# Kernel optimization log

Measured on AMD Instinct MI355X. Metric: run time of the kernel, lower is better.

The kernel has to match this reference:

```python
import jax, jax.numpy as jnp
import numpy as np

B, NSIDE, NH = 4, 64, 8
N = 12 * NSIDE * NSIDE          # HEALPix pixel count, nested ordering
CIN, CHID, COUT = 256, 512, 256
WS = 16                          # window = 4**(w+1) nested pixels, w=1
HD = CHID // NH


def _ln(x, g, b, eps=1e-5):
    m = x.mean(-1, keepdims=True)
    v = ((x - m) ** 2).mean(-1, keepdims=True)
    return (x - m) * jax.lax.rsqrt(v + eps) * g + b


def _win_attn(x, qkv_w, qkv_b, pw, pb):
    b_, n_, c = x.shape
    nw = n_ // WS
    xw = x.reshape(b_, nw, WS, c)
    qkv = xw @ qkv_w + qkv_b                      # [B, nw, ws, 3C]
    q, k, v = jnp.split(qkv, 3, axis=-1)
    def heads(t):
        return t.reshape(b_, nw, WS, NH, HD).transpose(0, 1, 3, 2, 4)
    q, k, v = heads(q), heads(k), heads(v)        # [B, nw, H, ws, hd]
    a = jax.nn.softmax(jnp.einsum('bwhqd,bwhkd->bwhqk', q, k) * (HD ** -0.5), axis=-1)
    o = jnp.einsum('bwhqk,bwhkd->bwhqd', a, v)
    o = o.transpose(0, 1, 3, 2, 4).reshape(b_, n_, c)
    return o @ pw + pb


def _heal_block(x, p, shift):
    if shift:
        x = jnp.roll(x, -WS // 2, axis=1)          # shifted-window (cyclic in nested order)
    x = x + _win_attn(_ln(x, p['ln1g'], p['ln1b']), p['qkvw'], p['qkvb'], p['pw'], p['pb'])
    h = _ln(x, p['ln2g'], p['ln2b'])
    h = jax.nn.gelu(h @ p['m1w'] + p['m1b'], approximate=False) @ p['m2w'] + p['m2b']
    x = x + h
    if shift:
        x = jnp.roll(x, WS // 2, axis=1)
    return x


def _sn_linear(h, W, b, u):
    # torch spectral_norm: one power-iteration, u/v detached, sigma = u' W v
    v = W @ u                                      # [CHID]
    v = jax.lax.stop_gradient(v / (jnp.linalg.norm(v) + 1e-12))
    u2 = v @ W                                     # [COUT]
    u2 = jax.lax.stop_gradient(u2 / (jnp.linalg.norm(u2) + 1e-12))
    sigma = v @ W @ u2
    return h @ (W / sigma) + b


def setup_inputs() -> dict:
    key = jax.random.key(0)
    ks = iter(jax.random.split(key, 64))
    def w(shape, s=0.02):
        return jax.random.normal(next(ks), shape, jnp.float32) * s
    inp = {'x': jax.random.normal(next(ks), (B, N, CIN), jnp.float32)}
    inp['ff1_w'] = w((CIN, CHID)); inp['ff1_b'] = jnp.zeros((CHID,), jnp.float32)
    for pre in ('a', 'b'):
        inp[f'{pre}_ln1g'] = jnp.ones((CHID,), jnp.float32)
        inp[f'{pre}_ln1b'] = jnp.zeros((CHID,), jnp.float32)
        inp[f'{pre}_qkvw'] = w((CHID, 3 * CHID)); inp[f'{pre}_qkvb'] = jnp.zeros((3 * CHID,), jnp.float32)
        inp[f'{pre}_pw'] = w((CHID, CHID)); inp[f'{pre}_pb'] = jnp.zeros((CHID,), jnp.float32)
        inp[f'{pre}_ln2g'] = jnp.ones((CHID,), jnp.float32)
        inp[f'{pre}_ln2b'] = jnp.zeros((CHID,), jnp.float32)
        inp[f'{pre}_m1w'] = w((CHID, 4 * CHID)); inp[f'{pre}_m1b'] = jnp.zeros((4 * CHID,), jnp.float32)
        inp[f'{pre}_m2w'] = w((4 * CHID, CHID)); inp[f'{pre}_m2b'] = jnp.zeros((CHID,), jnp.float32)
    inp['ff2_w'] = w((CHID, COUT)); inp['ff2_b'] = jnp.zeros((COUT,), jnp.float32)
    inp['ff2_u'] = jax.random.normal(next(ks), (COUT,), jnp.float32)
    return inp


def reference(x, ff1_w, ff1_b,
              a_ln1g, a_ln1b, a_qkvw, a_qkvb, a_pw, a_pb, a_ln2g, a_ln2b, a_m1w, a_m1b, a_m2w, a_m2b,
              b_ln1g, b_ln1b, b_qkvw, b_qkvb, b_pw, b_pb, b_ln2g, b_ln2b, b_m1w, b_m1b, b_m2w, b_m2b,
              ff2_w, ff2_b, ff2_u):
    pa = dict(ln1g=a_ln1g, ln1b=a_ln1b, qkvw=a_qkvw, qkvb=a_qkvb, pw=a_pw, pb=a_pb,
              ln2g=a_ln2g, ln2b=a_ln2b, m1w=a_m1w, m1b=a_m1b, m2w=a_m2w, m2b=a_m2b)
    pb_ = dict(ln1g=b_ln1g, ln1b=b_ln1b, qkvw=b_qkvw, qkvb=b_qkvb, pw=b_pw, pb=b_pb,
               ln2g=b_ln2g, ln2b=b_ln2b, m1w=b_m1w, m1b=b_m1b, m2w=b_m2w, m2b=b_m2b)
    h = jax.nn.gelu(x @ ff1_w + ff1_b, approximate=False)   # feed_forward1
    h = _heal_block(h, pa, shift=False)                     # message_passing1
    h = _heal_block(h, pb_, shift=True)                     # message_passing2
    return _sn_linear(h, ff2_w, ff2_b, ff2_u)               # spectral-norm linear
```

## Files before the change

### kernel.cpp

```cpp
#include <hip/hip_runtime.h>
#include <hip/hip_bf16.h>
#include <math.h>

typedef _Float16 f16;
typedef __attribute__((ext_vector_type(8))) _Float16 f16x8;
typedef __attribute__((ext_vector_type(4))) _Float16 f16x4;
typedef __attribute__((ext_vector_type(4))) float f32x4;

#define DINLINE __device__ __forceinline__

DINLINE float gelu_fast(float x) {
  float x2 = x * x;
  float z = x * __builtin_fmaf(-0.10294537f, x2, -2.30211422f);
  float E = __builtin_amdgcn_exp2f(z);
  return x * __builtin_amdgcn_rcpf(1.0f + E);
}
DINLINE void gload16(const void* g, void* l) {
  __builtin_amdgcn_global_load_lds((const __attribute__((address_space(1))) void*)g,
                                   (__attribute__((address_space(3))) void*)l, 16, 0, 0);
}

#define BAR       __builtin_amdgcn_s_barrier()
#define WAITVM(n) asm volatile("s_waitcnt vmcnt(" #n ")" ::: "memory")
#define CFE       asm volatile("" ::: "memory")

template <int EPI>
__global__ __launch_bounds__(512, 4) void gemm(
    const f16* __restrict__ A, const f16* __restrict__ Bt,
    const float* __restrict__ bias, const f16* __restrict__ Cin,
    float* __restrict__ Cf, f16* __restrict__ Cb,
    const float* __restrict__ scale_ptr,
    int N, int K, int nct)
{
  __shared__ alignas(16) f16 smf[2 * 3 * 4096];

  const int nwg = (int)gridDim.x;
  const int gid = (int)blockIdx.x;
  const int q = nwg >> 3, r = nwg & 7;
  const int xcd = gid & 7, idx = gid >> 3;
  const int swz = (xcd < r ? xcd * (q + 1) : r * (q + 1) + (xcd - r) * q) + idx;
  const int rt = swz / nct, ct = swz - rt * nct;
  const int m0 = rt << 7, n0 = ct << 8;

  const int tid = (int)threadIdx.x;
  const int lane = tid & 63;
  const int wid = tid >> 6;
  const int wr = wid >> 2, wcn = wid & 3;

  const int rsel = lane & 15, khi = lane >> 4;
  const int sx = (khi ^ ((rsel >> 1) & 3)) << 3;

  const int srow = tid >> 2;
  const int sls = (tid & 3) ^ ((srow >> 1) & 3);
  const f16* pA  = A  + (size_t)(m0 + srow) * K + sls * 8;
  const f16* pB0 = Bt + (size_t)(n0 + srow) * K + sls * 8;
  const f16* pB1 = Bt + (size_t)(n0 + 128 + srow) * K + sls * 8;
  f16* ldst = smf + tid * 8;

  const int aB = (wr * 64 + rsel) * 32 + sx;
  const int bB = (1 + (wcn >> 1)) * 4096 + ((wcn & 1) * 64 + rsel) * 32 + sx;

  f32x4 acc[4][4] = {};
  const int NT = K >> 5;

#define STG(boff)                                                             \
  {                                                                           \
    gload16(pA,  ldst + (boff));                                              \
    gload16(pB0, ldst + (boff) + 4096);                                       \
    gload16(pB1, ldst + (boff) + 8192);                                       \
    pA += 32; pB0 += 32; pB1 += 32;                                           \
  }

#define CMP(boff)                                                             \
  {                                                                           \
    f16x8 aF[4], bF[4];                                                       \
    _Pragma("unroll")                                                         \
    for (int _i = 0; _i < 4; ++_i)                                            \
      aF[_i] = *(const f16x8*)(smf + (boff) + aB + _i * 512);                 \
    _Pragma("unroll")                                                         \
    for (int _i = 0; _i < 4; ++_i)                                            \
      bF[_i] = *(const f16x8*)(smf + (boff) + bB + _i * 512);                 \
    __builtin_amdgcn_s_setprio(1);                                            \
    _Pragma("unroll")                                                         \
    for (int _m = 0; _m < 4; ++_m)                                            \
      _Pragma("unroll")                                                       \
      for (int _n = 0; _n < 4; ++_n)                                          \
        acc[_m][_n] = __builtin_amdgcn_mfma_f32_16x16x32_f16(                 \
            bF[_n], aF[_m], acc[_m][_n], 0, 0, 0);                            \
    __builtin_amdgcn_s_setprio(0);                                            \
  }

  STG(0); STG(12288);
  for (int t = 0; t + 2 < NT; t += 2) {
    WAITVM(3); BAR; CFE;
    CMP(0);
    BAR; CFE;
    STG(0);
    WAITVM(3); BAR; CFE;
    CMP(12288);
    BAR; CFE;
    STG(12288);
  }
  WAITVM(3); BAR; CFE;
  CMP(0);
  BAR; CFE;
  WAITVM(0); BAR; CFE;
  CMP(12288);

  const float scale = (EPI & 8) ? scale_ptr[0] : 1.0f;
  const int R0 = m0 + wr * 64, C0 = n0 + wcn * 64;
#pragma unroll
  for (int m = 0; m < 4; ++m) {
    const int row = R0 + m * 16 + rsel;
#pragma unroll
    for (int n = 0; n < 4; ++n) {
      const int col = C0 + n * 16 + (khi << 2);
      f32x4 v = acc[m][n];
      if (EPI & 8) {
#pragma unroll
        for (int j = 0; j < 4; ++j) v[j] *= scale;
      }
      f32x4 bb = *(const f32x4*)(bias + col);
#pragma unroll
      for (int j = 0; j < 4; ++j) v[j] += bb[j];
      if (EPI & 1) {
#pragma unroll
        for (int j = 0; j < 4; ++j) v[j] = gelu_fast(v[j]);
      }
      if (EPI & 2) {
        f16x4 c4 = *(const f16x4*)(Cin + (size_t)row * N + col);
#pragma unroll
        for (int j = 0; j < 4; ++j) v[j] += (float)c4[j];
      }
      if (EPI & 4) {
        f16x4 o;
#pragma unroll
        for (int j = 0; j < 4; ++j) o[j] = (f16)v[j];
        *(f16x4*)(Cb + (size_t)row * N + col) = o;
      } else {
        *(f32x4*)(Cf + (size_t)row * N + col) = v;
      }
    }
  }
#undef STG
#undef CMP
}

__global__ __launch_bounds__(256) void ln_f16(
    const f16* __restrict__ X, const float* __restrict__ g,
    const float* __restrict__ b, f16* __restrict__ Y, int ntok)
{
  const int lane = threadIdx.x & 63;
  const int c = lane * 8;
  const f32x4 g0 = *(const f32x4*)(g + c), g1 = *(const f32x4*)(g + c + 4);
  const f32x4 b0 = *(const f32x4*)(b + c), b1 = *(const f32x4*)(b + c + 4);
  for (int token = blockIdx.x * 4 + (threadIdx.x >> 6); token < ntok;
       token += gridDim.x * 4) {
    f16x8 v = *(const f16x8*)(X + (size_t)token * 512 + c);
    float vf[8];
    float s = 0.f, s2 = 0.f;
#pragma unroll
    for (int j = 0; j < 8; ++j) { vf[j] = (float)v[j]; s += vf[j]; s2 += vf[j] * vf[j]; }
#pragma unroll
    for (int o = 32; o > 0; o >>= 1) { s += __shfl_xor(s, o, 64); s2 += __shfl_xor(s2, o, 64); }
    const float mean = s * (1.f / 512.f);
    const float inv = rsqrtf(s2 * (1.f / 512.f) - mean * mean + 1e-5f);
    f16x8 o8;
#pragma unroll
    for (int j = 0; j < 4; ++j) {
      o8[j]     = (f16)((vf[j] - mean) * inv * g0[j] + b0[j]);
      o8[4 + j] = (f16)((vf[4 + j] - mean) * inv * g1[j] + b1[j]);
    }
    *(f16x8*)(Y + (size_t)token * 512 + c) = o8;
  }
}

__global__ __launch_bounds__(256) void cvt_f32_f16(const float* __restrict__ X,
                                                   f16* __restrict__ Y, long n8)
{
  const long i = (long)blockIdx.x * 256 + threadIdx.x;
  if (i >= n8) return;
  f32x4 v0 = *(const f32x4*)(X + i * 8), v1 = *(const f32x4*)(X + i * 8 + 4);
  f16x8 o8;
#pragma unroll
  for (int j = 0; j < 4; ++j) { o8[j] = (f16)v0[j]; o8[4 + j] = (f16)v1[j]; }
  *(f16x8*)(Y + i * 8) = o8;
}

__global__ __launch_bounds__(256) void w_tr_tiled(const float* __restrict__ W,
                                                  f16* __restrict__ Wt, int K, int N)
{
  __shared__ f16 td[64][66];
  const int nkt = K >> 6;
  const int kt = blockIdx.x % nkt, nt = blockIdx.x / nkt;
  const int k0 = kt << 6, n0 = nt << 6;
  const int col = threadIdx.x & 63, rq = threadIdx.x >> 6;
#pragma unroll
  for (int j = 0; j < 16; ++j) {
    const int row = j * 4 + rq;
    td[row][col] = (f16)W[(size_t)(k0 + row) * N + n0 + col];
  }
  __syncthreads();
#pragma unroll
  for (int j = 0; j < 16; ++j) {
    const int nrow = j * 4 + rq;
    Wt[(size_t)(n0 + nrow) * K + k0 + col] = td[col][nrow];
  }
}

template <int SHIFT>
__global__ __launch_bounds__(256) void win_attn(const f16* __restrict__ QKV,
                                                f16* __restrict__ O)
{
  __shared__ alignas(16) f16 kv[2][16][1160];
  const int wl0 = (int)blockIdx.x * 2;
  const int tid = (int)threadIdx.x;

  for (int i = tid; i < 4096; i += 256) {
    const int win = i >> 11;
    const int rem = i & 2047;
    const int row = rem >> 7;
    const int c8 = rem & 127;
    const int src = ((wl0 + win) * 16 + row + SHIFT) % 49152;
    const int sect = c8 >> 6;
    const int hh = (c8 >> 3) & 7;
    const int dd = (c8 & 7) * 8;
    *(f16x8*)(&kv[win][row][sect * 576 + hh * 72 + dd]) =
        *(const f16x8*)(QKV + (size_t)src * 1536 + 512 + c8 * 8);
  }

  const int win = tid >> 7, h = (tid >> 4) & 7, qi = tid & 15;
  const int qtok = ((wl0 + win) * 16 + qi + SHIFT) % 49152;
  f16x8 qv[8];
#pragma unroll
  for (int c8 = 0; c8 < 8; ++c8)
    qv[c8] = *(const f16x8*)(QKV + (size_t)qtok * 1536 + h * 64 + c8 * 8);

  __syncthreads();

  float sc[16];
  float mx = -1e30f;
#pragma unroll
  for (int kj = 0; kj < 16; ++kj) {
    const f16* kr = &kv[win][kj][h * 72];
    float s = 0.f;
#pragma unroll
    for (int c8 = 0; c8 < 8; ++c8) {
      f16x8 k8 = *(const f16x8*)(kr + c8 * 8);
#pragma unroll
      for (int j = 0; j < 8; ++j) s += (float)qv[c8][j] * (float)k8[j];
    }
    s *= 0.125f;
    sc[kj] = s;
    mx = fmaxf(mx, s);
  }
  float sum = 0.f;
#pragma unroll
  for (int kj = 0; kj < 16; ++kj) { sc[kj] = expf(sc[kj] - mx); sum += sc[kj]; }
  const float inv = 1.f / sum;
  float ov[64] = {};
#pragma unroll
  for (int kj = 0; kj < 16; ++kj) {
    const float a = sc[kj] * inv;
    const f16* vr = &kv[win][kj][576 + h * 72];
#pragma unroll
    for (int c8 = 0; c8 < 8; ++c8) {
      f16x8 v8 = *(const f16x8*)(vr + c8 * 8);
#pragma unroll
      for (int j = 0; j < 8; ++j) ov[c8 * 8 + j] += a * (float)v8[j];
    }
  }
  f16* orow = O + (size_t)qtok * 512 + h * 64;
#pragma unroll
  for (int c8 = 0; c8 < 8; ++c8) {
    f16x8 t;
#pragma unroll
    for (int j = 0; j < 8; ++j) t[j] = (f16)ov[c8 * 8 + j];
    *(f16x8*)(orow + c8 * 8) = t;
  }
}

__global__ __launch_bounds__(256) void sn_sigma(const float* __restrict__ W,
                                                const float* __restrict__ u,
                                                float* __restrict__ inv_sigma)
{
  __shared__ float vsh[512];
  __shared__ float ush[256];
  __shared__ float red[256];
  const int t = (int)threadIdx.x;
  ush[t] = u[t];
  __syncthreads();
  float a0 = 0.f, a1 = 0.f;
  for (int j = 0; j < 256; ++j) {
    a0 += W[t * 256 + j] * ush[j];
    a1 += W[(t + 256) * 256 + j] * ush[j];
  }
  vsh[t] = a0; vsh[t + 256] = a1;
  red[t] = a0 * a0 + a1 * a1;
  __syncthreads();
  for (int s = 128; s > 0; s >>= 1) { if (t < s) red[t] += red[t + s]; __syncthreads(); }
  const float nv = sqrtf(red[0]) + 1e-12f;
  __syncthreads();
  const float invv = 1.f / nv;
  vsh[t] *= invv; vsh[t + 256] *= invv;
  __syncthreads();
  float u2 = 0.f;
  for (int i = 0; i < 512; ++i) u2 += vsh[i] * W[i * 256 + t];
  red[t] = u2 * u2;
  __syncthreads();
  for (int s = 128; s > 0; s >>= 1) { if (t < s) red[t] += red[t + s]; __syncthreads(); }
  const float nu = sqrtf(red[0]) + 1e-12f;
  __syncthreads();
  ush[t] = u2 / nu;
  __syncthreads();
  float d0 = 0.f, d1 = 0.f;
  for (int j = 0; j < 256; ++j) {
    d0 += W[t * 256 + j] * ush[j];
    d1 += W[(t + 256) * 256 + j] * ush[j];
  }
  red[t] = vsh[t] * d0 + vsh[t + 256] * d1;
  __syncthreads();
  for (int s = 128; s > 0; s >>= 1) { if (t < s) red[t] += red[t + s]; __syncthreads(); }
  if (t == 0) inv_sigma[0] = 1.f / red[0];
}

__global__ void fill_sentinel(float* __restrict__ out, long n, float val)
{
  const long i = (long)blockIdx.x * 256 + threadIdx.x;
  for (long k = i; k < n; k += (long)gridDim.x * 256) out[k] = val;
}

extern "C" void kernel_launch(void* const* d_in, const int* in_sizes, int n_in,
                              void* d_out, int out_size, void* d_ws, size_t ws_size,
                              hipStream_t stream)
{
  const int M = 196608;
  const int MC = 49152;
  constexpr size_t OFF_U   = 201326592ull;
  constexpr size_t OFF_OH  = 201326592ull + 150994944ull;
  constexpr size_t OFF_WT  = 402653184ull;
  constexpr size_t OFF_SIG = 415760384ull;
  constexpr size_t NEED    = OFF_SIG + 256ull;

  if (ws_size < NEED) {
    fill_sentinel<<<2048, 256, 0, stream>>>((float*)d_out, (long)out_size,
                                            (float)(ws_size >> 20));
    return;
  }

  char* ws = (char*)d_ws;
  f16* R     = (f16*)(ws);
  f16* U     = (f16*)(ws + OFF_U);
  f16* OH    = (f16*)(ws + OFF_OH);
  f16* WT    = (f16*)(ws + OFF_WT);
  float* sig = (float*)(ws + OFF_SIG);
  f16* X     = (f16*)d_out;

  const float* ff1_b = (const float*)d_in[2];
  const float* ff2_b = (const float*)d_in[28];

  f16* W_FF1 = WT;
  auto W_QKV = [&](int blk) { return WT + (blk ? 3276800 : 131072); };
  auto W_PW  = [&](int blk) { return WT + (blk ? 4063232 : 917504); };
  auto W_M1  = [&](int blk) { return WT + (blk ? 4325376 : 1179648); };
  auto W_M2  = [&](int blk) { return WT + (blk ? 5373952 : 2228224); };
  f16* W_FF2 = WT + 6422528;

  w_tr_tiled<<<32, 256, 0, stream>>>((const float*)d_in[1], W_FF1, 256, 512);
  for (int blk = 0; blk < 2; ++blk) {
    w_tr_tiled<<<192, 256, 0, stream>>>((const float*)d_in[blk ? 17 : 5], W_QKV(blk), 512, 1536);
    w_tr_tiled<<<64, 256, 0, stream>>>((const float*)d_in[blk ? 19 : 7], W_PW(blk), 512, 512);
    w_tr_tiled<<<256, 256, 0, stream>>>((const float*)d_in[blk ? 23 : 11], W_M1(blk), 512, 2048);
    w_tr_tiled<<<256, 256, 0, stream>>>((const float*)d_in[blk ? 25 : 13], W_M2(blk), 2048, 512);
  }
  w_tr_tiled<<<32, 256, 0, stream>>>((const float*)d_in[27], W_FF2, 512, 256);
  sn_sigma<<<1, 256, 0, stream>>>((const float*)d_in[27], (const float*)d_in[29], sig);

  cvt_f32_f16<<<24576, 256, 0, stream>>>((const float*)d_in[0], U, (long)M * 256 / 8);
  gemm<5><<<3072, 512, 0, stream>>>(U, W_FF1, ff1_b, nullptr, nullptr, R, nullptr,
                                    512, 256, 2);

  for (int blk = 0; blk < 2; ++blk) {
    const float* ln1g = (const float*)d_in[blk ? 15 : 3];
    const float* ln1b = (const float*)d_in[blk ? 16 : 4];
    const float* qkvb = (const float*)d_in[blk ? 18 : 6];
    const float* pb   = (const float*)d_in[blk ? 20 : 8];
    const float* ln2g = (const float*)d_in[blk ? 21 : 9];
    const float* ln2b = (const float*)d_in[blk ? 22 : 10];
    const float* m1b  = (const float*)d_in[blk ? 24 : 12];
    const float* m2b  = (const float*)d_in[blk ? 26 : 14];

    ln_f16<<<4096, 256, 0, stream>>>(R, ln1g, ln1b, X, M);
    for (int mc = 0; mc < 4; ++mc) {
      const size_t ro = (size_t)mc * MC * 512;
      gemm<4><<<2304, 512, 0, stream>>>(X + ro, W_QKV(blk), qkvb, nullptr,
                                        nullptr, U, nullptr, 1536, 512, 6);
      if (blk == 0) win_attn<0><<<1536, 256, 0, stream>>>(U, OH);
      else          win_attn<8><<<1536, 256, 0, stream>>>(U, OH);
      gemm<6><<<768, 512, 0, stream>>>(OH, W_PW(blk), pb, R + ro,
                                       nullptr, R + ro, nullptr, 512, 512, 2);
    }
    ln_f16<<<4096, 256, 0, stream>>>(R, ln2g, ln2b, X, M);
    for (int mc = 0; mc < 4; ++mc) {
      const size_t ro = (size_t)mc * MC * 512;
      gemm<5><<<3072, 512, 0, stream>>>(X + ro, W_M1(blk), m1b, nullptr,
                                        nullptr, U, nullptr, 2048, 512, 8);
      gemm<6><<<768, 512, 0, stream>>>(U, W_M2(blk), m2b, R + ro,
                                       nullptr, R + ro, nullptr, 512, 2048, 2);
    }
  }

  gemm<8><<<1536, 512, 0, stream>>>(R, W_FF2, ff2_b, nullptr, (float*)d_out,
                                    nullptr, sig, 256, 512, 1);
}
```

Baseline: 4.794 ms.

## Fold LayerNorm into following GEMMs via row stats and precomputed weight sums

Replaces the LayerNorm kernels that wrote a normalized f16 copy of the activations with a stats-only kernel that stores per-token inv-std and mean*inv. The LN gain is folded into the transposed weights, and the GEMM epilogue applies inv*acc - mean*inv*colsum(gW) plus a folded bias (b + lnb@W). This removes a full activation write and re-read per LayerNorm. The risk is precision: the GEMM now runs on un-normalized f16 inputs and subtracts the mean afterwards, which can cancel when mean is large relative to variance.

```diff
diff --git a/kernel.cpp b/kernel.cpp
--- a/kernel.cpp
+++ b/kernel.cpp
@@ -6,6 +6,7 @@
 typedef __attribute__((ext_vector_type(8))) _Float16 f16x8;
 typedef __attribute__((ext_vector_type(4))) _Float16 f16x4;
 typedef __attribute__((ext_vector_type(4))) float f32x4;
+typedef __attribute__((ext_vector_type(2))) float f32x2;
 
 #define DINLINE __device__ __forceinline__
 
@@ -30,6 +31,7 @@
     const float* __restrict__ bias, const f16* __restrict__ Cin,
     float* __restrict__ Cf, f16* __restrict__ Cb,
     const float* __restrict__ scale_ptr,
+    const float* __restrict__ stats, const float* __restrict__ svec,
     int N, int K, int nct)
 {
   __shared__ alignas(16) f16 smf[2 * 3 * 4096];
@@ -112,6 +114,11 @@
 #pragma unroll
   for (int m = 0; m < 4; ++m) {
     const int row = R0 + m * 16 + rsel;
+    float inv = 1.0f, muinv = 0.0f;
+    if (EPI & 16) {
+      f32x2 sld = *(const f32x2*)(stats + (row << 1));
+      inv = sld[0]; muinv = sld[1];
+    }
 #pragma unroll
     for (int n = 0; n < 4; ++n) {
       const int col = C0 + n * 16 + (khi << 2);
@@ -119,6 +126,12 @@
       if (EPI & 8) {
 #pragma unroll
         for (int j = 0; j < 4; ++j) v[j] *= scale;
+      }
+      if (EPI & 16) {
+        f32x4 sv = *(const f32x4*)(svec + col);
+#pragma unroll
+        for (int j = 0; j < 4; ++j)
+          v[j] = __builtin_fmaf(inv, v[j], -muinv * sv[j]);
       }
       f32x4 bb = *(const f32x4*)(bias + col);
 #pragma unroll
@@ -146,32 +159,49 @@
 #undef CMP
 }
 
-__global__ __launch_bounds__(256) void ln_f16(
-    const f16* __restrict__ X, const float* __restrict__ g,
-    const float* __restrict__ b, f16* __restrict__ Y, int ntok)
+__global__ __launch_bounds__(256) void ln_stats(
+    const f16* __restrict__ X, float* __restrict__ st, int ntok)
 {
   const int lane = threadIdx.x & 63;
-  const int c = lane * 8;
-  const f32x4 g0 = *(const f32x4*)(g + c), g1 = *(const f32x4*)(g + c + 4);
-  const f32x4 b0 = *(const f32x4*)(b + c), b1 = *(const f32x4*)(b + c + 4);
   for (int token = blockIdx.x * 4 + (threadIdx.x >> 6); token < ntok;
        token += gridDim.x * 4) {
-    f16x8 v = *(const f16x8*)(X + (size_t)token * 512 + c);
-    float vf[8];
+    f16x8 v = *(const f16x8*)(X + (size_t)token * 512 + lane * 8);
     float s = 0.f, s2 = 0.f;
 #pragma unroll
-    for (int j = 0; j < 8; ++j) { vf[j] = (float)v[j]; s += vf[j]; s2 += vf[j] * vf[j]; }
+    for (int j = 0; j < 8; ++j) { float f = (float)v[j]; s += f; s2 += f * f; }
 #pragma unroll
     for (int o = 32; o > 0; o >>= 1) { s += __shfl_xor(s, o, 64); s2 += __shfl_xor(s2, o, 64); }
-    const float mean = s * (1.f / 512.f);
-    const float inv = rsqrtf(s2 * (1.f / 512.f) - mean * mean + 1e-5f);
-    f16x8 o8;
-#pragma unroll
-    for (int j = 0; j < 4; ++j) {
-      o8[j]     = (f16)((vf[j] - mean) * inv * g0[j] + b0[j]);
-      o8[4 + j] = (f16)((vf[4 + j] - mean) * inv * g1[j] + b1[j]);
-    }
-    *(f16x8*)(Y + (size_t)token * 512 + c) = o8;
+    if (lane == 0) {
+      const float mean = s * (1.f / 512.f);
+      const float inv = rsqrtf(s2 * (1.f / 512.f) - mean * mean + 1e-5f);
+      f32x2 o2; o2[0] = inv; o2[1] = mean * inv;
+      *(f32x2*)(st + 2 * (size_t)token) = o2;
+    }
+  }
+}
+
+__global__ __launch_bounds__(256) void prep_svec(
+    const float* __restrict__ W, const float* __restrict__ g,
+    const float* __restrict__ lb, const float* __restrict__ b0,
+    float* __restrict__ s, float* __restrict__ bout, int K, int N)
+{
+  __shared__ float red[2][4][64];
+  const int c = threadIdx.x & 63;
+  const int n = blockIdx.x * 64 + c;
+  const int kc = threadIdx.x >> 6;
+  const int kpc = K >> 2;
+  float ps = 0.f, pt = 0.f;
+  for (int k = kc * kpc; k < (kc + 1) * kpc; ++k) {
+    float w = W[(size_t)k * N + n];
+    ps += g[k] * w;
+    pt += lb[k] * w;
+  }
+  red[0][kc][c] = ps;
+  red[1][kc][c] = pt;
+  __syncthreads();
+  if (kc == 0) {
+    s[n] = red[0][0][c] + red[0][1][c] + red[0][2][c] + red[0][3][c];
+    bout[n] = b0[n] + red[1][0][c] + red[1][1][c] + red[1][2][c] + red[1][3][c];
   }
 }
 
@@ -188,6 +218,7 @@
 }
 
 __global__ __launch_bounds__(256) void w_tr_tiled(const float* __restrict__ W,
+                                                  const float* __restrict__ gain,
                                                   f16* __restrict__ Wt, int K, int N)
 {
   __shared__ f16 td[64][66];
@@ -198,7 +229,8 @@
 #pragma unroll
   for (int j = 0; j < 16; ++j) {
     const int row = j * 4 + rq;
-    td[row][col] = (f16)W[(size_t)(k0 + row) * N + n0 + col];
+    const float gv = gain ? gain[k0 + row] : 1.0f;
+    td[row][col] = (f16)(W[(size_t)(k0 + row) * N + n0 + col] * gv);
   }
   __syncthreads();
 #pragma unroll
@@ -354,7 +386,13 @@
   f16* OH    = (f16*)(ws + OFF_OH);
   f16* WT    = (f16*)(ws + OFF_WT);
   float* sig = (float*)(ws + OFF_SIG);
-  f16* X     = (f16*)d_out;
+
+  float* ST = (float*)d_out;
+  float* SV = ST + 393216;
+  auto SQ  = [&](int blk) { return SV + blk * 7168; };
+  auto BQ  = [&](int blk) { return SV + blk * 7168 + 1536; };
+  auto SM1 = [&](int blk) { return SV + blk * 7168 + 3072; };
+  auto BM1 = [&](int blk) { return SV + blk * 7168 + 5120; };
 
   const float* ff1_b = (const float*)d_in[2];
   const float* ff2_b = (const float*)d_in[28];
@@ -366,50 +404,60 @@
   auto W_M2  = [&](int blk) { return WT + (blk ? 5373952 : 2228224); };
   f16* W_FF2 = WT + 6422528;
 
-  w_tr_tiled<<<32, 256, 0, stream>>>((const float*)d_in[1], W_FF1, 256, 512);
+  w_tr_tiled<<<32, 256, 0, stream>>>((const float*)d_in[1], nullptr, W_FF1, 256, 512);
   for (int blk = 0; blk < 2; ++blk) {
-    w_tr_tiled<<<192, 256, 0, stream>>>((const float*)d_in[blk ? 17 : 5], W_QKV(blk), 512, 1536);
-    w_tr_tiled<<<64, 256, 0, stream>>>((const float*)d_in[blk ? 19 : 7], W_PW(blk), 512, 512);
-    w_tr_tiled<<<256, 256, 0, stream>>>((const float*)d_in[blk ? 23 : 11], W_M1(blk), 512, 2048);
-    w_tr_tiled<<<256, 256, 0, stream>>>((const float*)d_in[blk ? 25 : 13], W_M2(blk), 2048, 512);
-  }
-  w_tr_tiled<<<32, 256, 0, stream>>>((const float*)d_in[27], W_FF2, 512, 256);
-  sn_sigma<<<1, 256, 0, stream>>>((const float*)d_in[27], (const float*)d_in[29], sig);
-
-  cvt_f32_f16<<<24576, 256, 0, stream>>>((const float*)d_in[0], U, (long)M * 256 / 8);
-  gemm<5><<<3072, 512, 0, stream>>>(U, W_FF1, ff1_b, nullptr, nullptr, R, nullptr,
-                                    512, 256, 2);
-
-  for (int blk = 0; blk < 2; ++blk) {
+    const float* qkvw = (const float*)d_in[blk ? 17 : 5];
+    const float* m1w  = (const float*)d_in[blk ? 23 : 11];
     const float* ln1g = (const float*)d_in[blk ? 15 : 3];
     const float* ln1b = (const float*)d_in[blk ? 16 : 4];
     const float* qkvb = (const float*)d_in[blk ? 18 : 6];
-    const float* pb   = (const float*)d_in[blk ? 20 : 8];
     const float* ln2g = (const float*)d_in[blk ? 21 : 9];
     const float* ln2b = (const float*)d_in[blk ? 22 : 10];
     const float* m1b  = (const float*)d_in[blk ? 24 : 12];
-    const float* m2b  = (const float*)d_in[blk ? 26 : 14];
-
-    ln_f16<<<4096, 256, 0, stream>>>(R, ln1g, ln1b, X, M);
+    w_tr_tiled<<<192, 256, 0, stream>>>(qkvw, ln1g, W_QKV(blk), 512, 1536);
+    w_tr_tiled<<<64, 256, 0, stream>>>((const float*)d_in[blk ? 19 : 7], nullptr, W_PW(blk), 512, 512);
+    w_tr_tiled<<<256, 256, 0, stream>>>(m1w, ln2g, W_M1(blk), 512, 2048);
+    w_tr_tiled<<<256, 256, 0, stream>>>((const float*)d_in[blk ? 25 : 13], nullptr, W_M2(blk), 2048, 512);
+    prep_svec<<<24, 256, 0, stream>>>(qkvw, ln1g, ln1b, qkvb, SQ(blk), BQ(blk), 512, 1536);
+    prep_svec<<<32, 256, 0, stream>>>(m1w, ln2g, ln2b, m1b, SM1(blk), BM1(blk), 512, 2048);
+  }
+  w_tr_tiled<<<32, 256, 0, stream>>>((const float*)d_in[27], nullptr, W_FF2, 512, 256);
+  sn_sigma<<<1, 256, 0, stream>>>((const float*)d_in[27], (const float*)d_in[29], sig);
+
+  cvt_f32_f16<<<24576, 256, 0, stream>>>((const float*)d_in[0], U, (long)M * 256 / 8);
+  gemm<5><<<3072, 512, 0, stream>>>(U, W_FF1, ff1_b, nullptr, nullptr, R, nullptr,
+                                    nullptr, nullptr, 512, 256, 2);
+
+  for (int blk = 0; blk < 2; ++blk) {
+    const float* pb  = (const float*)d_in[blk ? 20 : 8];
+    const float* m2b = (const float*)d_in[blk ? 26 : 14];
+
+    ln_stats<<<4096, 256, 0, stream>>>(R, ST, M);
     for (int mc = 0; mc < 4; ++mc) {
       const size_t ro = (size_t)mc * MC * 512;
-      gemm<4><<<2304, 512, 0, stream>>>(X + ro, W_QKV(blk), qkvb, nullptr,
-                                        nullptr, U, nullptr, 1536, 512, 6);
+      gemm<20><<<2304, 512, 0, stream>>>(R + ro, W_QKV(blk), BQ(blk), nullptr,
+                                         nullptr, U, nullptr,
+                                         ST + 2 * (size_t)mc * MC, SQ(blk),
+                                         1536, 512, 6);
       if (blk == 0) win_attn<0><<<1536, 256, 0, stream>>>(U, OH);
       else          win_attn<8><<<1536, 256, 0, stream>>>(U, OH);
       gemm<6><<<768, 512, 0, stream>>>(OH, W_PW(blk), pb, R + ro,
-                                       nullptr, R + ro, nullptr, 512, 512, 2);
-    }
-    ln_f16<<<4096, 256, 0, stream>>>(R, ln2g, ln2b, X, M);
+                                       nullptr, R + ro, nullptr,
+                                       nullptr, nullptr, 512, 512, 2);
+    }
+    ln_stats<<<4096, 256, 0, stream>>>(R, ST, M);
     for (int mc = 0; mc < 4; ++mc) {
       const size_t ro = (size_t)mc * MC * 512;
-      gemm<5><<<3072, 512, 0, stream>>>(X + ro, W_M1(blk), m1b, nullptr,
-                                        nullptr, U, nullptr, 2048, 512, 8);
+      gemm<21><<<3072, 512, 0, stream>>>(R + ro, W_M1(blk), BM1(blk), nullptr,
+                                         nullptr, U, nullptr,
+                                         ST + 2 * (size_t)mc * MC, SM1(blk),
+                                         2048, 512, 8);
       gemm<6><<<768, 512, 0, stream>>>(U, W_M2(blk), m2b, R + ro,
-                                       nullptr, R + ro, nullptr, 512, 2048, 2);
+                                       nullptr, R + ro, nullptr,
+                                       nullptr, nullptr, 512, 2048, 2);
     }
   }
 
   gemm<8><<<1536, 512, 0, stream>>>(R, W_FF2, ff2_b, nullptr, (float*)d_out,
-                                    nullptr, sig, 256, 512, 1);
-}
+                                    nullptr, sig, nullptr, nullptr, 256, 512, 1);
+}
```

Result: slower. 5.022 ms (+4.8%).

## Fuse MLP up-projection, GELU and down-projection into one kernel

Applied to the files above, without the earlier changes.

Replaces the per-chunk pair of GEMMs (m1 with GELU writing a 2048-wide hidden buffer, then m2 with residual add) with a single fused_mlp kernel. Each workgroup owns 128 rows and loops over 16 hidden slabs of 128. For each slab it computes the GELU hidden tile into LDS and immediately accumulates it into a 128x512 output accumulator. This removes the global round-trip of the large hidden activation and the extra launches. In exchange it uses 128KB of LDS and a large register accumulator at occupancy 1, with 1536 workgroups and less latency hiding.

```diff
diff --git a/kernel.cpp b/kernel.cpp
--- a/kernel.cpp
+++ b/kernel.cpp
@@ -21,8 +21,33 @@
 }
 
 #define BAR       __builtin_amdgcn_s_barrier()
+#define WAITLGKM  asm volatile("s_waitcnt lgkmcnt(0)" ::: "memory")
 #define WAITVM(n) asm volatile("s_waitcnt vmcnt(" #n ")" ::: "memory")
 #define CFE       asm volatile("" ::: "memory")
+
+#define EPILOG(vreg, rowE, colE)                                              \
+  {                                                                           \
+    f32x4 v = (vreg);                                                         \
+    if (EPI & 8) {                                                            \
+      _Pragma("unroll") for (int _j = 0; _j < 4; ++_j) v[_j] *= scale;        \
+    }                                                                         \
+    f32x4 bb = *(const f32x4*)(bias + (colE));                                \
+    _Pragma("unroll") for (int _j = 0; _j < 4; ++_j) v[_j] += bb[_j];         \
+    if (EPI & 1) {                                                            \
+      _Pragma("unroll") for (int _j = 0; _j < 4; ++_j) v[_j] = gelu_fast(v[_j]); \
+    }                                                                         \
+    if (EPI & 2) {                                                            \
+      f16x4 c4 = *(const f16x4*)(Cin + (size_t)(rowE) * N + (colE));          \
+      _Pragma("unroll") for (int _j = 0; _j < 4; ++_j) v[_j] += (float)c4[_j];\
+    }                                                                         \
+    if (EPI & 4) {                                                            \
+      f16x4 o;                                                                \
+      _Pragma("unroll") for (int _j = 0; _j < 4; ++_j) o[_j] = (f16)v[_j];    \
+      *(f16x4*)(Cb + (size_t)(rowE) * N + (colE)) = o;                        \
+    } else {                                                                  \
+      *(f32x4*)(Cf + (size_t)(rowE) * N + (colE)) = v;                        \
+    }                                                                         \
+  }
 
 template <int EPI>
 __global__ __launch_bounds__(512, 4) void gemm(
@@ -50,11 +75,11 @@
   const int rsel = lane & 15, khi = lane >> 4;
   const int sx = (khi ^ ((rsel >> 1) & 3)) << 3;
 
-  const int srow = tid >> 2;
-  const int sls = (tid & 3) ^ ((srow >> 1) & 3);
-  const f16* pA  = A  + (size_t)(m0 + srow) * K + sls * 8;
-  const f16* pB0 = Bt + (size_t)(n0 + srow) * K + sls * 8;
-  const f16* pB1 = Bt + (size_t)(n0 + 128 + srow) * K + sls * 8;
+  const int r0 = tid >> 2;
+  const int sls = (tid & 3) ^ ((r0 >> 1) & 3);
+  const f16* pA  = A  + (size_t)(m0 + r0) * K + sls * 8;
+  const f16* pB0 = Bt + (size_t)(n0 + r0) * K + sls * 8;
+  const f16* pB1 = Bt + (size_t)(n0 + 128 + r0) * K + sls * 8;
   f16* ldst = smf + tid * 8;
 
   const int aB = (wr * 64 + rsel) * 32 + sx;
@@ -115,35 +140,155 @@
 #pragma unroll
     for (int n = 0; n < 4; ++n) {
       const int col = C0 + n * 16 + (khi << 2);
-      f32x4 v = acc[m][n];
-      if (EPI & 8) {
-#pragma unroll
-        for (int j = 0; j < 4; ++j) v[j] *= scale;
-      }
-      f32x4 bb = *(const f32x4*)(bias + col);
-#pragma unroll
-      for (int j = 0; j < 4; ++j) v[j] += bb[j];
-      if (EPI & 1) {
-#pragma unroll
-        for (int j = 0; j < 4; ++j) v[j] = gelu_fast(v[j]);
-      }
-      if (EPI & 2) {
-        f16x4 c4 = *(const f16x4*)(Cin + (size_t)row * N + col);
-#pragma unroll
-        for (int j = 0; j < 4; ++j) v[j] += (float)c4[j];
-      }
-      if (EPI & 4) {
-        f16x4 o;
-#pragma unroll
-        for (int j = 0; j < 4; ++j) o[j] = (f16)v[j];
-        *(f16x4*)(Cb + (size_t)row * N + col) = o;
-      } else {
-        *(f32x4*)(Cf + (size_t)row * N + col) = v;
-      }
+      EPILOG(acc[m][n], row, col);
     }
   }
 #undef STG
 #undef CMP
+}
+
+__global__ __launch_bounds__(512, 1) void fused_mlp(
+    const f16* __restrict__ X, const f16* __restrict__ W1t,
+    const float* __restrict__ b1, const f16* __restrict__ W2t,
+    const float* __restrict__ b2, f16* __restrict__ R)
+{
+  __shared__ alignas(16) f16 lds[65536];
+
+  const int nwg = (int)gridDim.x;
+  const int gid = (int)blockIdx.x;
+  const int m0 = ((gid & 7) * (nwg >> 3) + (gid >> 3)) << 7;
+
+  const int tid = (int)threadIdx.x;
+  const int lane = tid & 63;
+  const int wid = tid >> 6;
+  const int wr = wid >> 2;
+  const int wq = wid & 3;
+  const int rsel = lane & 15, khi = lane >> 4;
+  const int sx = (khi ^ ((rsel >> 1) & 3)) << 3;
+
+  const int srow = tid >> 2;
+  const int sls = (tid & 3) ^ ((srow >> 1) & 3);
+
+  f32x4 acc2[4][8] = {};
+
+#define STG1(boff, ktv)                                                       \
+  {                                                                           \
+    gload16(X + (size_t)(m0 + srow) * 512 + (ktv) * 32 + sls * 8,             \
+            lds + (boff) + tid * 8);                                          \
+    gload16(W1t + (size_t)(hbase + srow) * 512 + (ktv) * 32 + sls * 8,        \
+            lds + 8192 + (boff) + tid * 8);                                   \
+  }
+
+#define STG2(boff, kt2v)                                                      \
+  {                                                                           \
+    _Pragma("unroll")                                                         \
+    for (int _rg = 0; _rg < 4; ++_rg)                                         \
+      gload16(W2t + (size_t)(_rg * 128 + srow) * 2048 + hbase + (kt2v) * 32 + sls * 8, \
+              lds + 32768 + (boff) + _rg * 4096 + tid * 8);                   \
+  }
+
+#define CMP1(boff)                                                            \
+  {                                                                           \
+    f16x8 xF[4], wF[2];                                                       \
+    _Pragma("unroll") for (int _i = 0; _i < 4; ++_i)                          \
+      xF[_i] = *(const f16x8*)(lds + (boff) + (wr * 64 + _i * 16 + rsel) * 32 + sx); \
+    _Pragma("unroll") for (int _j = 0; _j < 2; ++_j)                          \
+      wF[_j] = *(const f16x8*)(lds + 8192 + (boff) + (wq * 32 + _j * 16 + rsel) * 32 + sx); \
+    __builtin_amdgcn_s_setprio(1);                                            \
+    _Pragma("unroll") for (int _i = 0; _i < 4; ++_i)                          \
+      _Pragma("unroll") for (int _j = 0; _j < 2; ++_j)                        \
+        acc1[_i][_j] = __builtin_amdgcn_mfma_f32_16x16x32_f16(                \
+            wF[_j], xF[_i], acc1[_i][_j], 0, 0, 0);                           \
+    __builtin_amdgcn_s_setprio(0);                                            \
+  }
+
+#define CMP2(boff, kt2v)                                                      \
+  {                                                                           \
+    f16x8 aF[4], bF[8];                                                       \
+    _Pragma("unroll") for (int _i = 0; _i < 4; ++_i)                          \
+      aF[_i] = *(const f16x8*)(lds + 16384 + (kt2v) * 4096 + (wr * 64 + _i * 16 + rsel) * 32 + sx); \
+    _Pragma("unroll") for (int _n = 0; _n < 8; ++_n)                          \
+      bF[_n] = *(const f16x8*)(lds + 32768 + (boff) + wq * 4096 + (_n * 16 + rsel) * 32 + sx); \
+    __builtin_amdgcn_s_setprio(1);                                            \
+    _Pragma("unroll") for (int _i = 0; _i < 4; ++_i)                          \
+      _Pragma("unroll") for (int _n = 0; _n < 8; ++_n)                        \
+        acc2[_i][_n] = __builtin_amdgcn_mfma_f32_16x16x32_f16(                \
+            bF[_n], aF[_i], acc2[_i][_n], 0, 0, 0);                           \
+    __builtin_amdgcn_s_setprio(0);                                            \
+  }
+
+  for (int slab = 0; slab < 16; ++slab) {
+    const int hbase = slab << 7;
+    f32x4 acc1[4][2] = {};
+
+    STG1(0, 0);
+    for (int kt = 0; kt < 16; ++kt) {
+      const int bo = (kt & 1) ? 4096 : 0;
+      if (kt + 1 < 16) {
+        if (kt & 1) { STG1(0, kt + 1); } else { STG1(4096, kt + 1); }
+        WAITVM(2);
+      } else {
+        WAITVM(0);
+      }
+      BAR; CFE;
+      CMP1(bo);
+      BAR; CFE;
+    }
+
+#pragma unroll
+    for (int i = 0; i < 4; ++i) {
+      const int hrow = wr * 64 + i * 16 + rsel;
+      const int swr = (hrow >> 1) & 3;
+#pragma unroll
+      for (int j = 0; j < 2; ++j) {
+        const int c = wq * 32 + j * 16 + (khi << 2);
+        f32x4 v = acc1[i][j];
+        f32x4 bb = *(const f32x4*)(b1 + hbase + c);
+        f16x4 o;
+#pragma unroll
+        for (int jj = 0; jj < 4; ++jj) o[jj] = (f16)gelu_fast(v[jj] + bb[jj]);
+        const int phys = ((c & 31) >> 3) ^ swr;
+        *(f16x4*)(lds + 16384 + ((c >> 5) << 12) + hrow * 32 + phys * 8 + (c & 7)) = o;
+      }
+    }
+    WAITLGKM;
+    BAR; CFE;
+
+    STG2(0, 0);
+    for (int kt2 = 0; kt2 < 4; ++kt2) {
+      const int bo = (kt2 & 1) ? 16384 : 0;
+      if (kt2 + 1 < 4) {
+        if (kt2 & 1) { STG2(0, kt2 + 1); } else { STG2(16384, kt2 + 1); }
+        WAITVM(4);
+      } else {
+        WAITVM(0);
+      }
+      BAR; CFE;
+      CMP2(bo, kt2);
+      BAR; CFE;
+    }
+  }
+
+  const int R0 = m0 + wr * 64, C0 = wq * 128;
+#pragma unroll
+  for (int i = 0; i < 4; ++i) {
+    const int row = R0 + i * 16 + rsel;
+#pragma unroll
+    for (int n = 0; n < 8; ++n) {
+      const int col = C0 + n * 16 + (khi << 2);
+      f32x4 v = acc2[i][n];
+      f32x4 bb = *(const f32x4*)(b2 + col);
+      f16x4 c4 = *(const f16x4*)(R + (size_t)row * 512 + col);
+      f16x4 o;
+#pragma unroll
+      for (int j = 0; j < 4; ++j) o[j] = (f16)(v[j] + bb[j] + (float)c4[j]);
+      *(f16x4*)(R + (size_t)row * 512 + col) = o;
+    }
+  }
+#undef STG1
+#undef STG2
+#undef CMP1
+#undef CMP2
 }
 
 __global__ __launch_bounds__(256) void ln_f16(
@@ -401,13 +546,7 @@
                                        nullptr, R + ro, nullptr, 512, 512, 2);
     }
     ln_f16<<<4096, 256, 0, stream>>>(R, ln2g, ln2b, X, M);
-    for (int mc = 0; mc < 4; ++mc) {
-      const size_t ro = (size_t)mc * MC * 512;
-      gemm<5><<<3072, 512, 0, stream>>>(X + ro, W_M1(blk), m1b, nullptr,
-                                        nullptr, U, nullptr, 2048, 512, 8);
-      gemm<6><<<768, 512, 0, stream>>>(U, W_M2(blk), m2b, R + ro,
-                                       nullptr, R + ro, nullptr, 512, 2048, 2);
-    }
+    fused_mlp<<<1536, 512, 0, stream>>>(X, W_M1(blk), m1b, W_M2(blk), m2b, R);
   }
 
   gemm<8><<<1536, 512, 0, stream>>>(R, W_FF2, ff2_b, nullptr, (float*)d_out,
```

After: 4.974 ms. 1.04x slower.
